# Performance work log

Hardware: AMD Instinct MI355X
Metric: run time of the kernel (lower is better)

Reference implementation:

```python
import jax, jax.numpy as jnp
import numpy as np

N, E, D, R, G, C = 100000, 600000, 128, 4, 256, 16
EPS = 1e-5

def _rgcn(x, src, dst, edge_type, w_rel, w_root, b):
    # out_i = x_i @ W_root + b + sum_r mean_{j in N_r(i)} x_j @ W_r  (PyG RGCNConv, aggr='mean')
    x_src = x[src]                                   # [E, D] gather
    out = x @ w_root + b                             # [N, D]
    for r in range(R):
        m = (edge_type == r).astype(x.dtype)         # [E]
        msg = (x_src @ w_rel[r]) * m[:, None]        # [E, D]
        agg = jax.ops.segment_sum(msg, dst, num_segments=N)
        cnt = jax.ops.segment_sum(m, dst, num_segments=N)
        out = out + agg / jnp.maximum(cnt, 1.0)[:, None]
    return out

def _bn_eval(x, gamma, beta, mean, var):
    return (x - mean) * jax.lax.rsqrt(var + EPS) * gamma + beta

def setup_inputs() -> dict:
    key = jax.random.key(0)
    ks = jax.random.split(key, 12)
    x = jax.random.normal(ks[0], (N, D), dtype=jnp.float32)
    edge_index = jax.random.randint(ks[1], (2, E), 0, N)
    edge_type = jax.random.randint(ks[2], (E,), 0, R)
    batch = jnp.sort(jax.random.randint(ks[3], (N,), 0, G))
    s = 1.0 / np.sqrt(D)
    conv_rel_w = jax.random.normal(ks[4], (3, R, D, D), dtype=jnp.float32) * s
    conv_root_w = jax.random.normal(ks[5], (3, D, D), dtype=jnp.float32) * s
    conv_bias = jnp.zeros((3, D), dtype=jnp.float32)
    bn_gamma = jnp.ones((2, D), dtype=jnp.float32)
    bn_beta = jnp.zeros((2, D), dtype=jnp.float32)
    bn_mean = jax.random.normal(ks[6], (2, D), dtype=jnp.float32) * 0.1
    bn_var = jax.random.uniform(ks[7], (2, D), minval=0.5, maxval=1.5, dtype=jnp.float32)
    cls_w1 = jax.random.normal(ks[8], (D, D // 2), dtype=jnp.float32) * s
    cls_b1 = jnp.zeros((D // 2,), dtype=jnp.float32)
    cls_w2 = jax.random.normal(ks[9], (D // 2, C), dtype=jnp.float32) / np.sqrt(D // 2)
    cls_b2 = jnp.zeros((C,), dtype=jnp.float32)
    return {"x": x, "edge_index": edge_index, "edge_type": edge_type, "batch": batch,
            "conv_rel_w": conv_rel_w, "conv_root_w": conv_root_w, "conv_bias": conv_bias,
            "bn_gamma": bn_gamma, "bn_beta": bn_beta, "bn_mean": bn_mean, "bn_var": bn_var,
            "cls_w1": cls_w1, "cls_b1": cls_b1, "cls_w2": cls_w2, "cls_b2": cls_b2}

def reference(x, edge_index, edge_type, batch, conv_rel_w, conv_root_w, conv_bias,
              bn_gamma, bn_beta, bn_mean, bn_var, cls_w1, cls_b1, cls_w2, cls_b2):
    src, dst = edge_index[0], edge_index[1]
    prev = None
    h = x
    for i in range(3):
        h_new = _rgcn(h, src, dst, edge_type, conv_rel_w[i], conv_root_w[i], conv_bias[i])
        if prev is not None:
            h_new = h_new + prev  # residual (shapes always match: D==D)
        if i != 2:
            h_new = _bn_eval(h_new, bn_gamma[i], bn_beta[i], bn_mean[i], bn_var[i])
            h_new = jax.nn.elu(h_new)  # alpha=1; dropout inactive in eval
        prev = h_new
        h = h_new
    # global mean pool over graphs
    sums = jax.ops.segment_sum(h, batch, num_segments=G)          # [G, D]
    cnts = jax.ops.segment_sum(jnp.ones((N,), h.dtype), batch, num_segments=G)
    pooled = sums / jnp.maximum(cnts, 1.0)[:, None]
    z = jax.nn.elu(pooled @ cls_w1 + cls_b1)
    logits = z @ cls_w2 + cls_b2
    return jax.nn.log_softmax(logits, axis=-1)
```

## Files before the change

kernel.cpp:

```cpp
#include <hip/hip_runtime.h>
#include <hip/hip_bf16.h>

#define NN 100000
#define EE 600000
#define DD 128
#define GG 256
#define CCL 16

typedef __attribute__((ext_vector_type(8))) short short8;
typedef __attribute__((ext_vector_type(4))) float f32x4;
typedef const __attribute__((address_space(1))) void* gas_t;
typedef __attribute__((address_space(3))) void* las_t;

__device__ __forceinline__ void async_ld16(const void* g, void* l) {
    __builtin_amdgcn_global_load_lds((gas_t)g, (las_t)l, 16, 0, 0);
}
__device__ __forceinline__ unsigned short f2bf(float x) {
    unsigned u = __float_as_uint(x);
    unsigned r = (u + 0x7FFFu + ((u >> 16) & 1u)) >> 16;
    return (unsigned short)r;
}
__device__ __forceinline__ float bf2f(unsigned short b) {
    return __uint_as_float(((unsigned)b) << 16);
}
__device__ __forceinline__ void unpack8(uint4 v, float* f) {
    f[0] = __uint_as_float(v.x << 16); f[1] = __uint_as_float(v.x & 0xFFFF0000u);
    f[2] = __uint_as_float(v.y << 16); f[3] = __uint_as_float(v.y & 0xFFFF0000u);
    f[4] = __uint_as_float(v.z << 16); f[5] = __uint_as_float(v.z & 0xFFFF0000u);
    f[6] = __uint_as_float(v.w << 16); f[7] = __uint_as_float(v.w & 0xFFFF0000u);
}

__global__ __launch_bounds__(256) void sniff_kernel(const void* __restrict__ xraw, int* __restrict__ flag) {
    int t = threadIdx.x;
    const unsigned short* u = (const unsigned short*)xraw;
    int good = 0;
    #pragma unroll
    for (int i = 0; i < 4; i++) {
        unsigned short b = u[t * 4 + i];
        int e = (b >> 7) & 0xFF;
        if (e >= 107 && e <= 130) good++;
    }
    __shared__ int sg[256];
    sg[t] = good;
    __syncthreads();
    for (int s = 128; s > 0; s >>= 1) { if (t < s) sg[t] += sg[t + s]; __syncthreads(); }
    if (t == 0) flag[0] = (sg[0] >= 900) ? 1 : 0;
}

__device__ __forceinline__ float loadf(const void* p, size_t i, int isbf) {
    if (isbf) return bf2f(((const unsigned short*)p)[i]);
    return ((const float*)p)[i];
}

__global__ __launch_bounds__(256) void convx_kernel(const void* __restrict__ xraw, const int* __restrict__ flag,
                                                    __hip_bfloat16* __restrict__ xc) {
    int isbf = flag[0];
    size_t i0 = ((size_t)blockIdx.x * 256 + threadIdx.x) * 8;
    if (i0 >= (size_t)NN * DD) return;
    if (isbf) {
        *(uint4*)(xc + i0) = *(const uint4*)((const __hip_bfloat16*)xraw + i0);
    } else {
        const float* xf = (const float*)xraw;
        unsigned short o[8];
        #pragma unroll
        for (int j = 0; j < 8; j++) o[j] = f2bf(xf[i0 + j]);
        *(uint4*)(xc + i0) = *(uint4*)o;
    }
}

__global__ __launch_bounds__(256) void convw_kernel(const void* __restrict__ rel_raw, const void* __restrict__ root_raw,
                                                    const int* __restrict__ flag, __hip_bfloat16* __restrict__ wt) {
    int isbf = flag[0];
    int mat = blockIdx.x;
    int layer = mat / 5, g = mat % 5;
    size_t srcoff = (g == 0) ? (size_t)layer * 16384 : (size_t)(layer * 4 + (g - 1)) * 16384;
    const void* sraw = (g == 0) ? root_raw : rel_raw;
    __hip_bfloat16* dstp = wt + (size_t)mat * 16384;
    for (int idx = threadIdx.x; idx < 16384; idx += 256) {
        int k = idx >> 7, n = idx & 127;
        float v = loadf(sraw, srcoff + (size_t)k * 128 + n, isbf);
        dstp[n * 128 + k] = __float2bfloat16(v);
    }
}

__global__ __launch_bounds__(256) void convp_kernel(const void* bias, const void* bng, const void* bnb,
                                                    const void* bnm, const void* bnv, const void* w1,
                                                    const void* b1, const void* w2, const void* b2,
                                                    const int* __restrict__ flag, float* __restrict__ pf) {
    int isbf = flag[0];
    int b = blockIdx.x, t = threadIdx.x;
    if (b < 9) {
        const void* srcs[9] = {bias, bng, bnb, bnm, bnv, w1, b1, w2, b2};
        const int cnts[9] = {384, 256, 256, 256, 256, 8192, 64, 1024, 16};
        const int offs[9] = {0, 384, 640, 896, 1152, 1408, 9600, 9664, 10688};
        const void* s = srcs[b];
        int c = cnts[b], o = offs[b];
        for (int i = t; i < c; i += 256) pf[o + i] = loadf(s, i, isbf);
    } else {
        int bl = b - 9;
        if (t < 128) {
            float iva = rsqrtf(loadf(bnv, bl * 128 + t, isbf) + 1e-5f);
            float gm = loadf(bng, bl * 128 + t, isbf) * iva;
            float ga = loadf(bnb, bl * 128 + t, isbf) - loadf(bnm, bl * 128 + t, isbf) * gm;
            pf[11008 + bl * 256 + t] = gm;
            pf[11008 + bl * 256 + 128 + t] = ga;
        }
    }
}

__global__ __launch_bounds__(256) void count4_kernel(const int* __restrict__ dst, const int* __restrict__ et,
                                                     int* __restrict__ cnt4) {
    int e = blockIdx.x * 256 + threadIdx.x;
    if (e < EE) atomicAdd(&cnt4[dst[e] * 4 + et[e]], 1);
}

__global__ __launch_bounds__(256) void allocn_kernel(const int* __restrict__ cnt4, int* __restrict__ counter,
                                                     int* __restrict__ startn, int* __restrict__ wptr4) {
    int n = blockIdx.x * 256 + threadIdx.x;
    int lane = threadIdx.x & 63;
    int4 cv = make_int4(0, 0, 0, 0);
    int c = 0;
    if (n < NN) {
        cv = *(const int4*)(cnt4 + n * 4);
        c = cv.x + cv.y + cv.z + cv.w;
    }
    int v = c;
    #pragma unroll
    for (int d = 1; d < 64; d <<= 1) {
        int o = __shfl_up(v, d);
        if (lane >= d) v += o;
    }
    int base = 0;
    if (lane == 63) base = atomicAdd(counter, v);
    base = __shfl(base, 63);
    if (n < NN) {
        int s = base + v - c;
        startn[n] = s;
        wptr4[n * 4 + 0] = s;
        wptr4[n * 4 + 1] = s + cv.x;
        wptr4[n * 4 + 2] = s + cv.x + cv.y;
        wptr4[n * 4 + 3] = s + cv.x + cv.y + cv.z;
    }
}

__global__ __launch_bounds__(256) void fill4_kernel(const int* __restrict__ src, const int* __restrict__ dst,
                                                    const int* __restrict__ et, int* __restrict__ wptr4,
                                                    int* __restrict__ esrc) {
    int e = blockIdx.x * 256 + threadIdx.x;
    if (e < EE) {
        int pos = atomicAdd(&wptr4[dst[e] * 4 + et[e]], 1);
        esrc[pos] = src[e];
    }
}

__global__ __launch_bounds__(256) void agg_kernel(const __hip_bfloat16* __restrict__ h,
                                                  const int* __restrict__ esrc,
                                                  const int* __restrict__ startn,
                                                  const int* __restrict__ cnt4,
                                                  __hip_bfloat16* __restrict__ Abuf) {
    int node = blockIdx.x * 16 + (threadIdx.x >> 4);
    int c16 = threadIdx.x & 15;
    int col0 = c16 * 8;
    int4 cv = *(const int4*)(cnt4 + node * 4);
    int s = startn[node];
    int cr[4] = {cv.x, cv.y, cv.z, cv.w};
    #pragma unroll
    for (int r = 0; r < 4; r++) {
        int c = cr[r];
        float a[8];
        #pragma unroll
        for (int j = 0; j < 8; j++) a[j] = 0.f;
        int i = 0;
        for (; i + 4 <= c; i += 4) {
            int s4[4];
            uint4 vv[4];
            #pragma unroll
            for (int q = 0; q < 4; q++) s4[q] = esrc[s + i + q];
            #pragma unroll
            for (int q = 0; q < 4; q++) vv[q] = *(const uint4*)(h + (size_t)s4[q] * 128 + col0);
            #pragma unroll
            for (int q = 0; q < 4; q++) {
                float f[8];
                unpack8(vv[q], f);
                #pragma unroll
                for (int j = 0; j < 8; j++) a[j] += f[j];
            }
        }
        for (; i < c; i++) {
            int sq = esrc[s + i];
            uint4 v0 = *(const uint4*)(h + (size_t)sq * 128 + col0);
            float f[8];
            unpack8(v0, f);
            #pragma unroll
            for (int j = 0; j < 8; j++) a[j] += f[j];
        }
        float w = (c > 0) ? (1.f / (float)c) : 0.f;
        unsigned short u[8];
        #pragma unroll
        for (int j = 0; j < 8; j++) u[j] = f2bf(a[j] * w);
        *(uint4*)(Abuf + (size_t)node * 512 + r * 128 + col0) = *(uint4*)u;
        s += c;
    }
}

__global__ __launch_bounds__(256) void rgemm_kernel(const __hip_bfloat16* __restrict__ h_in,
                                                    const __hip_bfloat16* __restrict__ Abuf,
                                                    const __hip_bfloat16* __restrict__ wt5,
                                                    const float* __restrict__ bias,
                                                    const float* __restrict__ gmp,
                                                    const float* __restrict__ gap,
                                                    const __hip_bfloat16* __restrict__ hres,
                                                    __hip_bfloat16* __restrict__ hout,
                                                    int do_bn) {
    __shared__ __align__(16) short lds[16384];
    int t = threadIdx.x;
    int wave = t >> 6, lane = t & 63, quad = lane >> 4, r16 = lane & 15;
    int m0 = blockIdx.x * 128;

    int r0 = m0 + wave * 32 + r16;      if (r0 > NN - 1) r0 = NN - 1;
    int r1 = m0 + wave * 32 + 16 + r16; if (r1 > NN - 1) r1 = NN - 1;

    f32x4 acc[2][8];
    #pragma unroll
    for (int i = 0; i < 2; i++)
        #pragma unroll
        for (int j = 0; j < 8; j++) acc[i][j] = (f32x4){0.f, 0.f, 0.f, 0.f};

    #pragma unroll
    for (int ch = 0; ch < 5; ch++) {
        if (ch) __syncthreads();
        const __hip_bfloat16* wg = wt5 + (size_t)ch * 16384;
        #pragma unroll
        for (int j = 0; j < 8; j++) {
            int slot = j * 256 + t;
            int brow = slot >> 4, sp = slot & 15;
            async_ld16(wg + brow * 128 + (sp ^ (brow & 15)) * 8, &lds[slot * 8]);
        }
        const __hip_bfloat16* ap0;
        const __hip_bfloat16* ap1;
        if (ch == 0) {
            ap0 = h_in + (size_t)r0 * 128;
            ap1 = h_in + (size_t)r1 * 128;
        } else {
            ap0 = Abuf + (size_t)r0 * 512 + (ch - 1) * 128;
            ap1 = Abuf + (size_t)r1 * 512 + (ch - 1) * 128;
        }
        short8 a0[4], a1[4];
        #pragma unroll
        for (int kc = 0; kc < 4; kc++) {
            a0[kc] = *(const short8*)(ap0 + kc * 32 + quad * 8);
            a1[kc] = *(const short8*)(ap1 + kc * 32 + quad * 8);
        }
        __syncthreads();
        #pragma unroll
        for (int kc = 0; kc < 4; kc++) {
            int s = kc * 4 + quad;
            #pragma unroll
            for (int nt = 0; nt < 8; nt++) {
                int rb = nt * 16 + r16;
                short8 b = *(const short8*)&lds[(rb * 16 + (s ^ (rb & 15))) * 8];
                acc[0][nt] = __builtin_amdgcn_mfma_f32_16x16x32_bf16(a0[kc], b, acc[0][nt], 0, 0, 0);
                acc[1][nt] = __builtin_amdgcn_mfma_f32_16x16x32_bf16(a1[kc], b, acc[1][nt], 0, 0, 0);
            }
        }
    }

    float* cf = (float*)lds;
    #pragma unroll
    for (int half = 0; half < 2; half++) {
        __syncthreads();
        #pragma unroll
        for (int nt = half * 4; nt < half * 4 + 4; nt++) {
            int col = (nt - half * 4) * 16 + r16;
            #pragma unroll
            for (int mt = 0; mt < 2; mt++) {
                #pragma unroll
                for (int reg = 0; reg < 4; reg++) {
                    int crow = wave * 32 + mt * 16 + quad * 4 + reg;
                    cf[crow * 64 + col] = acc[mt][nt][reg];
                }
            }
        }
        __syncthreads();
        #pragma unroll
        for (int it = 0; it < 4; it++) {
            int u4 = it * 256 + t;
            int crow = u4 >> 3, seg = u4 & 7;
            int node = m0 + crow;
            if (node < NN) {
                int gcol0 = half * 64 + seg * 8;
                float a[8];
                #pragma unroll
                for (int j = 0; j < 8; j++) a[j] = cf[crow * 64 + seg * 8 + j] + bias[gcol0 + j];
                if (hres) {
                    float rf[8];
                    unpack8(*(const uint4*)(hres + (size_t)node * 128 + gcol0), rf);
                    #pragma unroll
                    for (int j = 0; j < 8; j++) a[j] += rf[j];
                }
                if (do_bn) {
                    #pragma unroll
                    for (int j = 0; j < 8; j++) {
                        float z = a[j] * gmp[gcol0 + j] + gap[gcol0 + j];
                        a[j] = z > 0.f ? z : expm1f(z);
                    }
                }
                unsigned short u[8];
                #pragma unroll
                for (int j = 0; j < 8; j++) u[j] = f2bf(a[j]);
                *(uint4*)(hout + (size_t)node * 128 + gcol0) = *(uint4*)u;
            }
        }
    }
}

__global__ __launch_bounds__(256) void pool_kernel(const __hip_bfloat16* __restrict__ h3,
                                                   const int* __restrict__ batch,
                                                   float* __restrict__ pooled) {
    int g = blockIdx.x, t = threadIdx.x;
    int rowpar = t >> 4, colg = t & 15;
    int lo = 0, hi = NN;
    while (lo < hi) { int mid = (lo + hi) >> 1; if (batch[mid] < g) lo = mid + 1; else hi = mid; }
    int s0 = lo;
    hi = NN;
    while (lo < hi) { int mid = (lo + hi) >> 1; if (batch[mid] < g + 1) lo = mid + 1; else hi = mid; }
    int s1 = lo;
    float a[8];
    #pragma unroll
    for (int j = 0; j < 8; j++) a[j] = 0.f;
    for (int n = s0 + rowpar; n < s1; n += 16) {
        float f[8];
        unpack8(*(const uint4*)(h3 + (size_t)n * 128 + colg * 8), f);
        #pragma unroll
        for (int j = 0; j < 8; j++) a[j] += f[j];
    }
    __shared__ float sd[16][128];
    #pragma unroll
    for (int j = 0; j < 8; j++) sd[rowpar][colg * 8 + j] = a[j];
    __syncthreads();
    if (t < 128) {
        float sum = 0.f;
        #pragma unroll
        for (int i = 0; i < 16; i++) sum += sd[i][t];
        int cgn = s1 - s0;
        pooled[g * 128 + t] = sum / (float)(cgn > 0 ? cgn : 1);
    }
}

__global__ __launch_bounds__(64) void cls_kernel(const float* __restrict__ pooled,
                                                 const float* __restrict__ pf,
                                                 const int* __restrict__ flag,
                                                 void* __restrict__ out) {
    int g = blockIdx.x, j = threadIdx.x;
    const float* w1 = pf + 1408;
    const float* b1 = pf + 9600;
    const float* w2 = pf + 9664;
    const float* b2 = pf + 10688;
    __shared__ float z[64];
    __shared__ float lg[16];
    const float* p = pooled + g * 128;
    float acc = b1[j];
    for (int d = 0; d < 128; d++) acc += p[d] * w1[d * 64 + j];
    acc = acc > 0.f ? acc : expm1f(acc);
    z[j] = acc;
    __syncthreads();
    if (j < CCL) {
        float l = b2[j];
        for (int k = 0; k < 64; k++) l += z[k] * w2[k * 16 + j];
        lg[j] = l;
    }
    __syncthreads();
    if (j < CCL) {
        float m = lg[0];
        for (int k = 1; k < CCL; k++) m = fmaxf(m, lg[k]);
        float s = 0.f;
        for (int k = 0; k < CCL; k++) s += expf(lg[k] - m);
        float val = lg[j] - m - logf(s);
        if (flag[0]) ((__hip_bfloat16*)out)[g * CCL + j] = __float2bfloat16(val);
        else         ((float*)out)[g * CCL + j] = val;
    }
}

extern "C" void kernel_launch(void* const* d_in, const int* in_sizes, int n_in,
                              void* d_out, int out_size, void* d_ws, size_t ws_size,
                              hipStream_t stream) {
    const void* x_raw    = d_in[0];
    const int* ei        = (const int*)d_in[1];
    const int* et        = (const int*)d_in[2];
    const int* batch     = (const int*)d_in[3];
    const void* rel_raw  = d_in[4];
    const void* root_raw = d_in[5];
    const int* srcp = ei;
    const int* dstp = ei + EE;

    char* ws = (char*)d_ws;
    size_t off = 0;
    auto take = [&](size_t bytes) { size_t r = off; off += (bytes + 1023) & ~(size_t)1023; return r; };
    __hip_bfloat16* Abuf  = (__hip_bfloat16*)(ws + take((size_t)NN * 512 * 2));
    __hip_bfloat16* xc    = (__hip_bfloat16*)(ws + take((size_t)NN * 128 * 2));
    __hip_bfloat16* hA    = (__hip_bfloat16*)(ws + take((size_t)NN * 128 * 2));
    __hip_bfloat16* hB    = (__hip_bfloat16*)(ws + take((size_t)NN * 128 * 2));
    __hip_bfloat16* hC    = (__hip_bfloat16*)(ws + take((size_t)NN * 128 * 2));
    __hip_bfloat16* wt    = (__hip_bfloat16*)(ws + take((size_t)15 * 16384 * 2));
    float* pf             = (float*)(ws + take((size_t)11520 * 4));
    float* pooled         = (float*)(ws + take((size_t)GG * 128 * 4));
    int* cnt4             = (int*)(ws + take((size_t)NN * 16 + 8));
    int* counter          = cnt4 + NN * 4;
    int* flag             = cnt4 + NN * 4 + 1;
    int* startn           = (int*)(ws + take((size_t)NN * 4));
    int* wptr4            = (int*)(ws + take((size_t)NN * 16));
    int* esrc             = (int*)(ws + take((size_t)EE * 4));

    hipMemsetAsync(cnt4, 0, (size_t)NN * 16 + 4, stream);
    sniff_kernel<<<1, 256, 0, stream>>>(x_raw, flag);
    convx_kernel<<<(NN * DD / 8 + 255) / 256, 256, 0, stream>>>(x_raw, flag, xc);
    convw_kernel<<<15, 256, 0, stream>>>(rel_raw, root_raw, flag, wt);
    convp_kernel<<<11, 256, 0, stream>>>(d_in[6], d_in[7], d_in[8], d_in[9], d_in[10],
                                         d_in[11], d_in[12], d_in[13], d_in[14], flag, pf);
    count4_kernel<<<(EE + 255) / 256, 256, 0, stream>>>(dstp, et, cnt4);
    allocn_kernel<<<(NN + 255) / 256, 256, 0, stream>>>(cnt4, counter, startn, wptr4);
    fill4_kernel<<<(EE + 255) / 256, 256, 0, stream>>>(srcp, dstp, et, wptr4, esrc);

    const __hip_bfloat16* hin = xc;
    __hip_bfloat16* houts[3] = {hA, hB, hC};
    for (int l = 0; l < 3; l++) {
        int bl = l < 2 ? l : 1;
        agg_kernel<<<NN / 16, 256, 0, stream>>>(hin, esrc, startn, cnt4, Abuf);
        rgemm_kernel<<<(NN + 127) / 128, 256, 0, stream>>>(
            hin, Abuf, wt + (size_t)l * 5 * 16384, pf + l * 128,
            pf + 11008 + bl * 256, pf + 11008 + bl * 256 + 128,
            (l > 0) ? hin : (const __hip_bfloat16*)nullptr, houts[l], (l < 2) ? 1 : 0);
        hin = houts[l];
    }
    pool_kernel<<<GG, 256, 0, stream>>>(houts[2], batch, pooled);
    cls_kernel<<<GG, 64, 0, stream>>>(pooled, pf, flag, (void*)d_out);
}
```

Measured before the change: 572.7 us.

## Double-buffer weight chunks and split rgemm across 8 waves

The fused relational GEMM now runs with 512 threads, so each of the 8 waves computes a 32x64 output tile instead of a 32x128 tile. Weight chunks are double-buffered in LDS and the next chunk's A rows are prefetched while the current chunk's MFMAs run, so loads overlap compute. The epilogue writes the whole 128-column tile to padded LDS (stride 132) in one pass instead of two halves. The cost is more LDS per block (about 66 KB) and extra registers for the prefetched A fragments, which may limit occupancy.

```diff
diff --git a/kernel.cpp b/kernel.cpp
--- a/kernel.cpp
+++ b/kernel.cpp
@@ -203,113 +203,113 @@
     }
 }
 
-__global__ __launch_bounds__(256) void rgemm_kernel(const __hip_bfloat16* __restrict__ h_in,
-                                                    const __hip_bfloat16* __restrict__ Abuf,
-                                                    const __hip_bfloat16* __restrict__ wt5,
-                                                    const float* __restrict__ bias,
-                                                    const float* __restrict__ gmp,
-                                                    const float* __restrict__ gap,
-                                                    const __hip_bfloat16* __restrict__ hres,
-                                                    __hip_bfloat16* __restrict__ hout,
-                                                    int do_bn) {
-    __shared__ __align__(16) short lds[16384];
+#define STAGE_B(P, CH) do { \
+    const __hip_bfloat16* _wg = wt5 + (size_t)(CH) * 16384; \
+    _Pragma("unroll") \
+    for (int _j = 0; _j < 4; _j++) { \
+        int _slot = _j * 512 + t; \
+        int _brow = _slot >> 4, _sp = _slot & 15; \
+        async_ld16(_wg + _brow * 128 + (_sp ^ (_brow & 15)) * 8, &ldsb[(P) * 16384 + _slot * 8]); \
+    } \
+} while (0)
+
+#define LOAD_A(D0, D1, CH) do { \
+    const __hip_bfloat16* _p0 = ((CH) == 0) ? (h_in + (size_t)r0 * 128) : (Abuf + (size_t)r0 * 512 + ((CH) - 1) * 128); \
+    const __hip_bfloat16* _p1 = ((CH) == 0) ? (h_in + (size_t)r1 * 128) : (Abuf + (size_t)r1 * 512 + ((CH) - 1) * 128); \
+    _Pragma("unroll") \
+    for (int _kc = 0; _kc < 4; _kc++) { \
+        D0[_kc] = *(const short8*)(_p0 + _kc * 32 + quad * 8); \
+        D1[_kc] = *(const short8*)(_p1 + _kc * 32 + quad * 8); \
+    } \
+} while (0)
+
+#define MFMA_CH(P, A0, A1) do { \
+    _Pragma("unroll") \
+    for (int _kc = 0; _kc < 4; _kc++) { \
+        int _s = _kc * 4 + quad; \
+        _Pragma("unroll") \
+        for (int _nt = 0; _nt < 4; _nt++) { \
+            int _rb = wc * 64 + _nt * 16 + r16; \
+            short8 _b = *(const short8*)&ldsb[(P) * 16384 + (_rb * 16 + (_s ^ (_rb & 15))) * 8]; \
+            acc0[_nt] = __builtin_amdgcn_mfma_f32_16x16x32_bf16(A0[_kc], _b, acc0[_nt], 0, 0, 0); \
+            acc1[_nt] = __builtin_amdgcn_mfma_f32_16x16x32_bf16(A1[_kc], _b, acc1[_nt], 0, 0, 0); \
+        } \
+    } \
+} while (0)
+
+__global__ __launch_bounds__(512, 4) void rgemm_kernel(const __hip_bfloat16* __restrict__ h_in,
+                                                       const __hip_bfloat16* __restrict__ Abuf,
+                                                       const __hip_bfloat16* __restrict__ wt5,
+                                                       const float* __restrict__ bias,
+                                                       const float* __restrict__ gmp,
+                                                       const float* __restrict__ gap,
+                                                       const __hip_bfloat16* __restrict__ hres,
+                                                       __hip_bfloat16* __restrict__ hout,
+                                                       int do_bn) {
+    __shared__ __align__(16) char ldsraw[132 * 128 * 4];
+    short* ldsb = (short*)ldsraw;
+    float* cf = (float*)ldsraw;
     int t = threadIdx.x;
     int wave = t >> 6, lane = t & 63, quad = lane >> 4, r16 = lane & 15;
+    int wr = wave & 3, wc = wave >> 2;
     int m0 = blockIdx.x * 128;
 
-    int r0 = m0 + wave * 32 + r16;      if (r0 > NN - 1) r0 = NN - 1;
-    int r1 = m0 + wave * 32 + 16 + r16; if (r1 > NN - 1) r1 = NN - 1;
-
-    f32x4 acc[2][8];
-    #pragma unroll
-    for (int i = 0; i < 2; i++)
-        #pragma unroll
-        for (int j = 0; j < 8; j++) acc[i][j] = (f32x4){0.f, 0.f, 0.f, 0.f};
-
-    #pragma unroll
-    for (int ch = 0; ch < 5; ch++) {
-        if (ch) __syncthreads();
-        const __hip_bfloat16* wg = wt5 + (size_t)ch * 16384;
-        #pragma unroll
-        for (int j = 0; j < 8; j++) {
-            int slot = j * 256 + t;
-            int brow = slot >> 4, sp = slot & 15;
-            async_ld16(wg + brow * 128 + (sp ^ (brow & 15)) * 8, &lds[slot * 8]);
+    int r0 = m0 + wr * 32 + r16;      if (r0 > NN - 1) r0 = NN - 1;
+    int r1 = m0 + wr * 32 + 16 + r16; if (r1 > NN - 1) r1 = NN - 1;
+
+    f32x4 acc0[4], acc1[4];
+    #pragma unroll
+    for (int j = 0; j < 4; j++) { acc0[j] = (f32x4){0.f, 0.f, 0.f, 0.f}; acc1[j] = (f32x4){0.f, 0.f, 0.f, 0.f}; }
+
+    short8 aA0[4], aA1[4], aB0[4], aB1[4];
+    LOAD_A(aA0, aA1, 0);
+    STAGE_B(0, 0);
+
+    __syncthreads();  STAGE_B(1, 1);  LOAD_A(aB0, aB1, 1);  MFMA_CH(0, aA0, aA1);
+    __syncthreads();  STAGE_B(0, 2);  LOAD_A(aA0, aA1, 2);  MFMA_CH(1, aB0, aB1);
+    __syncthreads();  STAGE_B(1, 3);  LOAD_A(aB0, aB1, 3);  MFMA_CH(0, aA0, aA1);
+    __syncthreads();  STAGE_B(0, 4);  LOAD_A(aA0, aA1, 4);  MFMA_CH(1, aB0, aB1);
+    __syncthreads();                                        MFMA_CH(0, aA0, aA1);
+
+    __syncthreads();
+    #pragma unroll
+    for (int nt = 0; nt < 4; nt++) {
+        int col = wc * 64 + nt * 16 + r16;
+        #pragma unroll
+        for (int reg = 0; reg < 4; reg++) {
+            int crow0 = wr * 32 + quad * 4 + reg;
+            cf[crow0 * 132 + col] = acc0[nt][reg];
+            cf[(crow0 + 16) * 132 + col] = acc1[nt][reg];
         }
-        const __hip_bfloat16* ap0;
-        const __hip_bfloat16* ap1;
-        if (ch == 0) {
-            ap0 = h_in + (size_t)r0 * 128;
-            ap1 = h_in + (size_t)r1 * 128;
-        } else {
-            ap0 = Abuf + (size_t)r0 * 512 + (ch - 1) * 128;
-            ap1 = Abuf + (size_t)r1 * 512 + (ch - 1) * 128;
-        }
-        short8 a0[4], a1[4];
-        #pragma unroll
-        for (int kc = 0; kc < 4; kc++) {
-            a0[kc] = *(const short8*)(ap0 + kc * 32 + quad * 8);
-            a1[kc] = *(const short8*)(ap1 + kc * 32 + quad * 8);
-        }
-        __syncthreads();
-        #pragma unroll
-        for (int kc = 0; kc < 4; kc++) {
-            int s = kc * 4 + quad;
-            #pragma unroll
-            for (int nt = 0; nt < 8; nt++) {
-                int rb = nt * 16 + r16;
-                short8 b = *(const short8*)&lds[(rb * 16 + (s ^ (rb & 15))) * 8];
-                acc[0][nt] = __builtin_amdgcn_mfma_f32_16x16x32_bf16(a0[kc], b, acc[0][nt], 0, 0, 0);
-                acc[1][nt] = __builtin_amdgcn_mfma_f32_16x16x32_bf16(a1[kc], b, acc[1][nt], 0, 0, 0);
+    }
+    __syncthreads();
+    #pragma unroll
+    for (int it = 0; it < 4; it++) {
+        int u4 = it * 512 + t;
+        int crow = u4 >> 4, seg = u4 & 15;
+        int node = m0 + crow;
+        if (node < NN) {
+            int gcol0 = seg * 8;
+            float a[8];
+            #pragma unroll
+            for (int j = 0; j < 8; j++) a[j] = cf[crow * 132 + gcol0 + j] + bias[gcol0 + j];
+            if (hres) {
+                float rf[8];
+                unpack8(*(const uint4*)(hres + (size_t)node * 128 + gcol0), rf);
+                #pragma unroll
+                for (int j = 0; j < 8; j++) a[j] += rf[j];
             }
-        }
-    }
-
-    float* cf = (float*)lds;
-    #pragma unroll
-    for (int half = 0; half < 2; half++) {
-        __syncthreads();
-        #pragma unroll
-        for (int nt = half * 4; nt < half * 4 + 4; nt++) {
-            int col = (nt - half * 4) * 16 + r16;
-            #pragma unroll
-            for (int mt = 0; mt < 2; mt++) {
+            if (do_bn) {
                 #pragma unroll
-                for (int reg = 0; reg < 4; reg++) {
-                    int crow = wave * 32 + mt * 16 + quad * 4 + reg;
-                    cf[crow * 64 + col] = acc[mt][nt][reg];
+                for (int j = 0; j < 8; j++) {
+                    float z = a[j] * gmp[gcol0 + j] + gap[gcol0 + j];
+                    a[j] = z > 0.f ? z : expm1f(z);
                 }
             }
-        }
-        __syncthreads();
-        #pragma unroll
-        for (int it = 0; it < 4; it++) {
-            int u4 = it * 256 + t;
-            int crow = u4 >> 3, seg = u4 & 7;
-            int node = m0 + crow;
-            if (node < NN) {
-                int gcol0 = half * 64 + seg * 8;
-                float a[8];
-                #pragma unroll
-                for (int j = 0; j < 8; j++) a[j] = cf[crow * 64 + seg * 8 + j] + bias[gcol0 + j];
-                if (hres) {
-                    float rf[8];
-                    unpack8(*(const uint4*)(hres + (size_t)node * 128 + gcol0), rf);
-                    #pragma unroll
-                    for (int j = 0; j < 8; j++) a[j] += rf[j];
-                }
-                if (do_bn) {
-                    #pragma unroll
-                    for (int j = 0; j < 8; j++) {
-                        float z = a[j] * gmp[gcol0 + j] + gap[gcol0 + j];
-                        a[j] = z > 0.f ? z : expm1f(z);
-                    }
-                }
-                unsigned short u[8];
-                #pragma unroll
-                for (int j = 0; j < 8; j++) u[j] = f2bf(a[j]);
-                *(uint4*)(hout + (size_t)node * 128 + gcol0) = *(uint4*)u;
-            }
+            unsigned short u[8];
+            #pragma unroll
+            for (int j = 0; j < 8; j++) u[j] = f2bf(a[j]);
+            *(uint4*)(hout + (size_t)node * 128 + gcol0) = *(uint4*)u;
         }
     }
 }
@@ -426,7 +426,7 @@
     for (int l = 0; l < 3; l++) {
         int bl = l < 2 ? l : 1;
         agg_kernel<<<NN / 16, 256, 0, stream>>>(hin, esrc, startn, cnt4, Abuf);
-        rgemm_kernel<<<(NN + 127) / 128, 256, 0, stream>>>(
+        rgemm_kernel<<<(NN + 127) / 128, 512, 0, stream>>>(
             hin, Abuf, wt + (size_t)l * 5 * 16384, pf + l * 128,
             pf + 11008 + bl * 256, pf + 11008 + bl * 256 + 128,
             (l > 0) ? hin : (const __hip_bfloat16*)nullptr, houts[l], (l < 2) ? 1 : 0);
```

Measured after the change: 651.9 us. 13.8% more time.

## Split GEMM over output-column halves with full-K weights in LDS; merge relation loops in aggregation

Applied to the files above, without the earlier changes.

The fused root+relation GEMM now uses a 2D grid that splits the 128 output columns into two halves. Each block loads its 64x640 weight slice into LDS once, with a new concatenated K=640 weight layout, instead of reloading five 128x128 chunks behind barriers. A-operands are preloaded into registers in two batches. The aggregation kernel walks all of a node's edges in one loop of 8 gathers, keeping four per-relation accumulators selected by masks, which exposes more memory-level parallelism. The costs are that A rows are now read twice (once per column half), LDS use grows to 80KB per block which lowers occupancy, and the aggregation does four times the FMAs per edge.

```diff
diff --git a/kernel.cpp b/kernel.cpp
--- a/kernel.cpp
+++ b/kernel.cpp
@@ -75,11 +75,11 @@
     int layer = mat / 5, g = mat % 5;
     size_t srcoff = (g == 0) ? (size_t)layer * 16384 : (size_t)(layer * 4 + (g - 1)) * 16384;
     const void* sraw = (g == 0) ? root_raw : rel_raw;
-    __hip_bfloat16* dstp = wt + (size_t)mat * 16384;
+    __hip_bfloat16* dstp = wt + (size_t)layer * 81920 + g * 128;
     for (int idx = threadIdx.x; idx < 16384; idx += 256) {
-        int k = idx >> 7, n = idx & 127;
-        float v = loadf(sraw, srcoff + (size_t)k * 128 + n, isbf);
-        dstp[n * 128 + k] = __float2bfloat16(v);
+        int kk = idx >> 7, n = idx & 127;
+        float v = loadf(sraw, srcoff + (size_t)kk * 128 + n, isbf);
+        dstp[(size_t)n * 640 + kk] = __float2bfloat16(v);
     }
 }
 
@@ -163,153 +163,181 @@
     int col0 = c16 * 8;
     int4 cv = *(const int4*)(cnt4 + node * 4);
     int s = startn[node];
-    int cr[4] = {cv.x, cv.y, cv.z, cv.w};
-    #pragma unroll
-    for (int r = 0; r < 4; r++) {
-        int c = cr[r];
-        float a[8];
-        #pragma unroll
-        for (int j = 0; j < 8; j++) a[j] = 0.f;
-        int i = 0;
-        for (; i + 4 <= c; i += 4) {
-            int s4[4];
-            uint4 vv[4];
+    int b1 = cv.x, b2 = b1 + cv.y, b3 = b2 + cv.z, ct = b3 + cv.w;
+    float a0[8], a1[8], a2[8], a3[8];
+    #pragma unroll
+    for (int j = 0; j < 8; j++) { a0[j] = 0.f; a1[j] = 0.f; a2[j] = 0.f; a3[j] = 0.f; }
+    int i = 0;
+    for (; i + 8 <= ct; i += 8) {
+        int e8[8];
+        uint4 vv[8];
+        #pragma unroll
+        for (int q = 0; q < 8; q++) e8[q] = esrc[s + i + q];
+        #pragma unroll
+        for (int q = 0; q < 8; q++) vv[q] = *(const uint4*)(h + (size_t)e8[q] * 128 + col0);
+        #pragma unroll
+        for (int q = 0; q < 8; q++) {
+            int pos = i + q;
+            int r = (pos >= b1) + (pos >= b2) + (pos >= b3);
+            float w0 = (r == 0) ? 1.f : 0.f, w1 = (r == 1) ? 1.f : 0.f;
+            float w2 = (r == 2) ? 1.f : 0.f, w3 = (r == 3) ? 1.f : 0.f;
+            float f[8];
+            unpack8(vv[q], f);
             #pragma unroll
-            for (int q = 0; q < 4; q++) s4[q] = esrc[s + i + q];
-            #pragma unroll
-            for (int q = 0; q < 4; q++) vv[q] = *(const uint4*)(h + (size_t)s4[q] * 128 + col0);
-            #pragma unroll
-            for (int q = 0; q < 4; q++) {
-                float f[8];
-                unpack8(vv[q], f);
-                #pragma unroll
-                for (int j = 0; j < 8; j++) a[j] += f[j];
+            for (int j = 0; j < 8; j++) {
+                a0[j] += w0 * f[j]; a1[j] += w1 * f[j];
+                a2[j] += w2 * f[j]; a3[j] += w3 * f[j];
             }
         }
-        for (; i < c; i++) {
-            int sq = esrc[s + i];
-            uint4 v0 = *(const uint4*)(h + (size_t)sq * 128 + col0);
-            float f[8];
-            unpack8(v0, f);
-            #pragma unroll
-            for (int j = 0; j < 8; j++) a[j] += f[j];
-        }
-        float w = (c > 0) ? (1.f / (float)c) : 0.f;
-        unsigned short u[8];
-        #pragma unroll
-        for (int j = 0; j < 8; j++) u[j] = f2bf(a[j] * w);
-        *(uint4*)(Abuf + (size_t)node * 512 + r * 128 + col0) = *(uint4*)u;
-        s += c;
-    }
+    }
+    for (; i < ct; i++) {
+        int e0 = esrc[s + i];
+        uint4 v0 = *(const uint4*)(h + (size_t)e0 * 128 + col0);
+        int r = (i >= b1) + (i >= b2) + (i >= b3);
+        float w0 = (r == 0) ? 1.f : 0.f, w1 = (r == 1) ? 1.f : 0.f;
+        float w2 = (r == 2) ? 1.f : 0.f, w3 = (r == 3) ? 1.f : 0.f;
+        float f[8];
+        unpack8(v0, f);
+        #pragma unroll
+        for (int j = 0; j < 8; j++) {
+            a0[j] += w0 * f[j]; a1[j] += w1 * f[j];
+            a2[j] += w2 * f[j]; a3[j] += w3 * f[j];
+        }
+    }
+    float i0 = 1.f / (float)(cv.x > 0 ? cv.x : 1);
+    float i1 = 1.f / (float)(cv.y > 0 ? cv.y : 1);
+    float i2 = 1.f / (float)(cv.z > 0 ? cv.z : 1);
+    float i3 = 1.f / (float)(cv.w > 0 ? cv.w : 1);
+    unsigned short u[8];
+    __hip_bfloat16* op = Abuf + (size_t)node * 512 + col0;
+    #pragma unroll
+    for (int j = 0; j < 8; j++) u[j] = f2bf(a0[j] * i0);
+    *(uint4*)(op) = *(uint4*)u;
+    #pragma unroll
+    for (int j = 0; j < 8; j++) u[j] = f2bf(a1[j] * i1);
+    *(uint4*)(op + 128) = *(uint4*)u;
+    #pragma unroll
+    for (int j = 0; j < 8; j++) u[j] = f2bf(a2[j] * i2);
+    *(uint4*)(op + 256) = *(uint4*)u;
+    #pragma unroll
+    for (int j = 0; j < 8; j++) u[j] = f2bf(a3[j] * i3);
+    *(uint4*)(op + 384) = *(uint4*)u;
 }
 
 __global__ __launch_bounds__(256) void rgemm_kernel(const __hip_bfloat16* __restrict__ h_in,
                                                     const __hip_bfloat16* __restrict__ Abuf,
-                                                    const __hip_bfloat16* __restrict__ wt5,
+                                                    const __hip_bfloat16* __restrict__ wtL,
                                                     const float* __restrict__ bias,
                                                     const float* __restrict__ gmp,
                                                     const float* __restrict__ gap,
                                                     const __hip_bfloat16* __restrict__ hres,
                                                     __hip_bfloat16* __restrict__ hout,
                                                     int do_bn) {
-    __shared__ __align__(16) short lds[16384];
+    __shared__ __align__(16) short ldsb[40960];
     int t = threadIdx.x;
-    int wave = t >> 6, lane = t & 63, quad = lane >> 4, r16 = lane & 15;
+    int wv = t >> 6, lane = t & 63, quad = lane >> 4, r16 = lane & 15;
     int m0 = blockIdx.x * 128;
-
-    int r0 = m0 + wave * 32 + r16;      if (r0 > NN - 1) r0 = NN - 1;
-    int r1 = m0 + wave * 32 + 16 + r16; if (r1 > NN - 1) r1 = NN - 1;
-
-    f32x4 acc[2][8];
-    #pragma unroll
-    for (int i = 0; i < 2; i++)
-        #pragma unroll
-        for (int j = 0; j < 8; j++) acc[i][j] = (f32x4){0.f, 0.f, 0.f, 0.f};
-
-    #pragma unroll
-    for (int ch = 0; ch < 5; ch++) {
-        if (ch) __syncthreads();
-        const __hip_bfloat16* wg = wt5 + (size_t)ch * 16384;
-        #pragma unroll
-        for (int j = 0; j < 8; j++) {
-            int slot = j * 256 + t;
-            int brow = slot >> 4, sp = slot & 15;
-            async_ld16(wg + brow * 128 + (sp ^ (brow & 15)) * 8, &lds[slot * 8]);
-        }
-        const __hip_bfloat16* ap0;
-        const __hip_bfloat16* ap1;
-        if (ch == 0) {
-            ap0 = h_in + (size_t)r0 * 128;
-            ap1 = h_in + (size_t)r1 * 128;
+    int nh = blockIdx.y;
+
+    #pragma unroll
+    for (int i = 0; i < 20; i++) {
+        int u = i * 256 + t;
+        int nl = u / 80;
+        int segp = u - nl * 80;
+        int seg = segp ^ (nl & 7);
+        async_ld16(wtL + (size_t)(nh * 64 + nl) * 640 + seg * 8, &ldsb[u * 8]);
+    }
+
+    int r0 = m0 + wv * 32 + r16;       if (r0 > NN - 1) r0 = NN - 1;
+    int r1 = m0 + wv * 32 + 16 + r16;  if (r1 > NN - 1) r1 = NN - 1;
+
+    short8 aA0[10], aA1[10];
+    #pragma unroll
+    for (int j = 0; j < 10; j++) {
+        if (j < 4) {
+            aA0[j] = *(const short8*)(h_in + (size_t)r0 * 128 + j * 32 + quad * 8);
+            aA1[j] = *(const short8*)(h_in + (size_t)r1 * 128 + j * 32 + quad * 8);
         } else {
-            ap0 = Abuf + (size_t)r0 * 512 + (ch - 1) * 128;
-            ap1 = Abuf + (size_t)r1 * 512 + (ch - 1) * 128;
-        }
-        short8 a0[4], a1[4];
-        #pragma unroll
-        for (int kc = 0; kc < 4; kc++) {
-            a0[kc] = *(const short8*)(ap0 + kc * 32 + quad * 8);
-            a1[kc] = *(const short8*)(ap1 + kc * 32 + quad * 8);
-        }
-        __syncthreads();
-        #pragma unroll
-        for (int kc = 0; kc < 4; kc++) {
-            int s = kc * 4 + quad;
+            aA0[j] = *(const short8*)(Abuf + (size_t)r0 * 512 + (j - 4) * 32 + quad * 8);
+            aA1[j] = *(const short8*)(Abuf + (size_t)r1 * 512 + (j - 4) * 32 + quad * 8);
+        }
+    }
+    __syncthreads();
+
+    short8 aB0[10], aB1[10];
+    #pragma unroll
+    for (int j = 0; j < 10; j++) {
+        aB0[j] = *(const short8*)(Abuf + (size_t)r0 * 512 + (j + 6) * 32 + quad * 8);
+        aB1[j] = *(const short8*)(Abuf + (size_t)r1 * 512 + (j + 6) * 32 + quad * 8);
+    }
+
+    f32x4 acc0[4], acc1[4];
+    #pragma unroll
+    for (int nt = 0; nt < 4; nt++) { acc0[nt] = (f32x4){0.f,0.f,0.f,0.f}; acc1[nt] = (f32x4){0.f,0.f,0.f,0.f}; }
+
+    #pragma unroll
+    for (int j = 0; j < 10; j++) {
+        #pragma unroll
+        for (int nt = 0; nt < 4; nt++) {
+            int nl = nt * 16 + r16;
+            int unit = nl * 80 + ((j * 4 + quad) ^ (nl & 7));
+            short8 b = *(const short8*)&ldsb[unit * 8];
+            acc0[nt] = __builtin_amdgcn_mfma_f32_16x16x32_bf16(aA0[j], b, acc0[nt], 0, 0, 0);
+            acc1[nt] = __builtin_amdgcn_mfma_f32_16x16x32_bf16(aA1[j], b, acc1[nt], 0, 0, 0);
+        }
+    }
+    #pragma unroll
+    for (int j = 0; j < 10; j++) {
+        #pragma unroll
+        for (int nt = 0; nt < 4; nt++) {
+            int nl = nt * 16 + r16;
+            int unit = nl * 80 + (((j + 10) * 4 + quad) ^ (nl & 7));
+            short8 b = *(const short8*)&ldsb[unit * 8];
+            acc0[nt] = __builtin_amdgcn_mfma_f32_16x16x32_bf16(aB0[j], b, acc0[nt], 0, 0, 0);
+            acc1[nt] = __builtin_amdgcn_mfma_f32_16x16x32_bf16(aB1[j], b, acc1[nt], 0, 0, 0);
+        }
+    }
+
+    __syncthreads();
+    float* cf = (float*)ldsb;
+    #pragma unroll
+    for (int nt = 0; nt < 4; nt++) {
+        int col = nt * 16 + r16;
+        #pragma unroll
+        for (int reg = 0; reg < 4; reg++) {
+            cf[(wv * 32 + quad * 4 + reg) * 66 + col] = acc0[nt][reg];
+            cf[(wv * 32 + 16 + quad * 4 + reg) * 66 + col] = acc1[nt][reg];
+        }
+    }
+    __syncthreads();
+    #pragma unroll
+    for (int it = 0; it < 4; it++) {
+        int u4 = it * 256 + t;
+        int row = u4 >> 3, oct = u4 & 7;
+        int onode = m0 + row;
+        if (onode < NN) {
+            int gc = nh * 64 + oct * 8;
+            const float* cp = cf + row * 66 + oct * 8;
+            float a[8];
             #pragma unroll
-            for (int nt = 0; nt < 8; nt++) {
-                int rb = nt * 16 + r16;
-                short8 b = *(const short8*)&lds[(rb * 16 + (s ^ (rb & 15))) * 8];
-                acc[0][nt] = __builtin_amdgcn_mfma_f32_16x16x32_bf16(a0[kc], b, acc[0][nt], 0, 0, 0);
-                acc[1][nt] = __builtin_amdgcn_mfma_f32_16x16x32_bf16(a1[kc], b, acc[1][nt], 0, 0, 0);
+            for (int j = 0; j < 8; j++) a[j] = cp[j] + bias[gc + j];
+            if (hres) {
+                float rf[8];
+                unpack8(*(const uint4*)(hres + (size_t)onode * 128 + gc), rf);
+                #pragma unroll
+                for (int j = 0; j < 8; j++) a[j] += rf[j];
             }
-        }
-    }
-
-    float* cf = (float*)lds;
-    #pragma unroll
-    for (int half = 0; half < 2; half++) {
-        __syncthreads();
-        #pragma unroll
-        for (int nt = half * 4; nt < half * 4 + 4; nt++) {
-            int col = (nt - half * 4) * 16 + r16;
-            #pragma unroll
-            for (int mt = 0; mt < 2; mt++) {
+            if (do_bn) {
                 #pragma unroll
-                for (int reg = 0; reg < 4; reg++) {
-                    int crow = wave * 32 + mt * 16 + quad * 4 + reg;
-                    cf[crow * 64 + col] = acc[mt][nt][reg];
+                for (int j = 0; j < 8; j++) {
+                    float z = a[j] * gmp[gc + j] + gap[gc + j];
+                    a[j] = z > 0.f ? z : expm1f(z);
                 }
             }
-        }
-        __syncthreads();
-        #pragma unroll
-        for (int it = 0; it < 4; it++) {
-            int u4 = it * 256 + t;
-            int crow = u4 >> 3, seg = u4 & 7;
-            int node = m0 + crow;
-            if (node < NN) {
-                int gcol0 = half * 64 + seg * 8;
-                float a[8];
-                #pragma unroll
-                for (int j = 0; j < 8; j++) a[j] = cf[crow * 64 + seg * 8 + j] + bias[gcol0 + j];
-                if (hres) {
-                    float rf[8];
-                    unpack8(*(const uint4*)(hres + (size_t)node * 128 + gcol0), rf);
-                    #pragma unroll
-                    for (int j = 0; j < 8; j++) a[j] += rf[j];
-                }
-                if (do_bn) {
-                    #pragma unroll
-                    for (int j = 0; j < 8; j++) {
-                        float z = a[j] * gmp[gcol0 + j] + gap[gcol0 + j];
-                        a[j] = z > 0.f ? z : expm1f(z);
-                    }
-                }
-                unsigned short u[8];
-                #pragma unroll
-                for (int j = 0; j < 8; j++) u[j] = f2bf(a[j]);
-                *(uint4*)(hout + (size_t)node * 128 + gcol0) = *(uint4*)u;
-            }
+            unsigned short u[8];
+            #pragma unroll
+            for (int j = 0; j < 8; j++) u[j] = f2bf(a[j]);
+            *(uint4*)(hout + (size_t)onode * 128 + gc) = *(uint4*)u;
         }
     }
 }
@@ -401,7 +429,7 @@
     __hip_bfloat16* hA    = (__hip_bfloat16*)(ws + take((size_t)NN * 128 * 2));
     __hip_bfloat16* hB    = (__hip_bfloat16*)(ws + take((size_t)NN * 128 * 2));
     __hip_bfloat16* hC    = (__hip_bfloat16*)(ws + take((size_t)NN * 128 * 2));
-    __hip_bfloat16* wt    = (__hip_bfloat16*)(ws + take((size_t)15 * 16384 * 2));
+    __hip_bfloat16* wt    = (__hip_bfloat16*)(ws + take((size_t)3 * 81920 * 2));
     float* pf             = (float*)(ws + take((size_t)11520 * 4));
     float* pooled         = (float*)(ws + take((size_t)GG * 128 * 4));
     int* cnt4             = (int*)(ws + take((size_t)NN * 16 + 8));
@@ -426,8 +454,8 @@
     for (int l = 0; l < 3; l++) {
         int bl = l < 2 ? l : 1;
         agg_kernel<<<NN / 16, 256, 0, stream>>>(hin, esrc, startn, cnt4, Abuf);
-        rgemm_kernel<<<(NN + 127) / 128, 256, 0, stream>>>(
-            hin, Abuf, wt + (size_t)l * 5 * 16384, pf + l * 128,
+        rgemm_kernel<<<dim3((NN + 127) / 128, 2), 256, 0, stream>>>(
+            hin, Abuf, wt + (size_t)l * 81920, pf + l * 128,
             pf + 11008 + bl * 256, pf + 11008 + bl * 256 + 128,
             (l > 0) ? hin : (const __hip_bfloat16*)nullptr, houts[l], (l < 2) ? 1 : 0);
         hin = houts[l];
```

Result: slower. 680.8 us (+18.9%).

## Read GEMM weights directly from global memory with a fused K=640 layout

Applied to the files above, without the earlier changes.

The weight conversion now writes each layer's five 128x128 matrices as one transposed [128 x 640] row-major block. The fused GEMM reads B fragments straight from global memory (cached in L2/L1) rather than staging each chunk into LDS with per-chunk barriers, and runs over the concatenated K dimension with a prefetch of the first aggregated chunk. This removes five LDS fills and their syncs per block, at the cost of more redundant global/cache loads per wave. The epilogue LDS tile is padded to stride 66 to reduce bank conflicts.

```diff
diff --git a/kernel.cpp b/kernel.cpp
--- a/kernel.cpp
+++ b/kernel.cpp
@@ -9,12 +9,7 @@
 
 typedef __attribute__((ext_vector_type(8))) short short8;
 typedef __attribute__((ext_vector_type(4))) float f32x4;
-typedef const __attribute__((address_space(1))) void* gas_t;
-typedef __attribute__((address_space(3))) void* las_t;
-
-__device__ __forceinline__ void async_ld16(const void* g, void* l) {
-    __builtin_amdgcn_global_load_lds((gas_t)g, (las_t)l, 16, 0, 0);
-}
+
 __device__ __forceinline__ unsigned short f2bf(float x) {
     unsigned u = __float_as_uint(x);
     unsigned r = (u + 0x7FFFu + ((u >> 16) & 1u)) >> 16;
@@ -75,11 +70,11 @@
     int layer = mat / 5, g = mat % 5;
     size_t srcoff = (g == 0) ? (size_t)layer * 16384 : (size_t)(layer * 4 + (g - 1)) * 16384;
     const void* sraw = (g == 0) ? root_raw : rel_raw;
-    __hip_bfloat16* dstp = wt + (size_t)mat * 16384;
+    __hip_bfloat16* dstp = wt + (size_t)layer * 81920 + g * 128;
     for (int idx = threadIdx.x; idx < 16384; idx += 256) {
-        int k = idx >> 7, n = idx & 127;
-        float v = loadf(sraw, srcoff + (size_t)k * 128 + n, isbf);
-        dstp[n * 128 + k] = __float2bfloat16(v);
+        int kk = idx >> 7, n = idx & 127;
+        float v = loadf(sraw, srcoff + (size_t)kk * 128 + n, isbf);
+        dstp[(size_t)n * 640 + kk] = __float2bfloat16(v);
     }
 }
 
@@ -205,110 +200,106 @@
 
 __global__ __launch_bounds__(256) void rgemm_kernel(const __hip_bfloat16* __restrict__ h_in,
                                                     const __hip_bfloat16* __restrict__ Abuf,
-                                                    const __hip_bfloat16* __restrict__ wt5,
+                                                    const __hip_bfloat16* __restrict__ wtL,
                                                     const float* __restrict__ bias,
                                                     const float* __restrict__ gmp,
                                                     const float* __restrict__ gap,
                                                     const __hip_bfloat16* __restrict__ hres,
                                                     __hip_bfloat16* __restrict__ hout,
                                                     int do_bn) {
-    __shared__ __align__(16) short lds[16384];
+    __shared__ __align__(16) float cf[128 * 66];
     int t = threadIdx.x;
-    int wave = t >> 6, lane = t & 63, quad = lane >> 4, r16 = lane & 15;
+    int wv = t >> 6, lane = t & 63, quad = lane >> 4, r16 = lane & 15;
     int m0 = blockIdx.x * 128;
-
-    int r0 = m0 + wave * 32 + r16;      if (r0 > NN - 1) r0 = NN - 1;
-    int r1 = m0 + wave * 32 + 16 + r16; if (r1 > NN - 1) r1 = NN - 1;
-
-    f32x4 acc[2][8];
-    #pragma unroll
-    for (int i = 0; i < 2; i++)
-        #pragma unroll
-        for (int j = 0; j < 8; j++) acc[i][j] = (f32x4){0.f, 0.f, 0.f, 0.f};
-
-    #pragma unroll
-    for (int ch = 0; ch < 5; ch++) {
-        if (ch) __syncthreads();
-        const __hip_bfloat16* wg = wt5 + (size_t)ch * 16384;
-        #pragma unroll
-        for (int j = 0; j < 8; j++) {
-            int slot = j * 256 + t;
-            int brow = slot >> 4, sp = slot & 15;
-            async_ld16(wg + brow * 128 + (sp ^ (brow & 15)) * 8, &lds[slot * 8]);
-        }
-        const __hip_bfloat16* ap0;
-        const __hip_bfloat16* ap1;
-        if (ch == 0) {
-            ap0 = h_in + (size_t)r0 * 128;
-            ap1 = h_in + (size_t)r1 * 128;
-        } else {
-            ap0 = Abuf + (size_t)r0 * 512 + (ch - 1) * 128;
-            ap1 = Abuf + (size_t)r1 * 512 + (ch - 1) * 128;
-        }
-        short8 a0[4], a1[4];
-        #pragma unroll
-        for (int kc = 0; kc < 4; kc++) {
-            a0[kc] = *(const short8*)(ap0 + kc * 32 + quad * 8);
-            a1[kc] = *(const short8*)(ap1 + kc * 32 + quad * 8);
-        }
-        __syncthreads();
-        #pragma unroll
-        for (int kc = 0; kc < 4; kc++) {
-            int s = kc * 4 + quad;
+    int r0 = m0 + wv * 32 + r16;      if (r0 > NN - 1) r0 = NN - 1;
+    int r1 = m0 + wv * 32 + 16 + r16; if (r1 > NN - 1) r1 = NN - 1;
+
+    f32x4 acc0[8], acc1[8];
+    #pragma unroll
+    for (int nt = 0; nt < 8; nt++) { acc0[nt] = (f32x4){0.f,0.f,0.f,0.f}; acc1[nt] = (f32x4){0.f,0.f,0.f,0.f}; }
+
+    const __hip_bfloat16* pb  = wtL + r16 * 640 + quad * 8;
+    const __hip_bfloat16* ph0 = h_in + (size_t)r0 * 128 + quad * 8;
+    const __hip_bfloat16* ph1 = h_in + (size_t)r1 * 128 + quad * 8;
+    const __hip_bfloat16* pa0 = Abuf + (size_t)r0 * 512 + quad * 8;
+    const __hip_bfloat16* pa1 = Abuf + (size_t)r1 * 512 + quad * 8;
+
+    short8 pf0 = *(const short8*)(pa0);
+    short8 pf1 = *(const short8*)(pa1);
+
+    #pragma unroll 2
+    for (int j = 0; j < 4; j++) {
+        short8 a0 = *(const short8*)(ph0 + j * 32);
+        short8 a1 = *(const short8*)(ph1 + j * 32);
+        #pragma unroll
+        for (int nt = 0; nt < 8; nt++) {
+            short8 b = *(const short8*)(pb + nt * 10240 + j * 32);
+            acc0[nt] = __builtin_amdgcn_mfma_f32_16x16x32_bf16(a0, b, acc0[nt], 0, 0, 0);
+            acc1[nt] = __builtin_amdgcn_mfma_f32_16x16x32_bf16(a1, b, acc1[nt], 0, 0, 0);
+        }
+    }
+    {
+        #pragma unroll
+        for (int nt = 0; nt < 8; nt++) {
+            short8 b = *(const short8*)(pb + nt * 10240 + 4 * 32);
+            acc0[nt] = __builtin_amdgcn_mfma_f32_16x16x32_bf16(pf0, b, acc0[nt], 0, 0, 0);
+            acc1[nt] = __builtin_amdgcn_mfma_f32_16x16x32_bf16(pf1, b, acc1[nt], 0, 0, 0);
+        }
+    }
+    #pragma unroll 2
+    for (int j = 1; j < 16; j++) {
+        short8 a0 = *(const short8*)(pa0 + j * 32);
+        short8 a1 = *(const short8*)(pa1 + j * 32);
+        #pragma unroll
+        for (int nt = 0; nt < 8; nt++) {
+            short8 b = *(const short8*)(pb + nt * 10240 + (j + 4) * 32);
+            acc0[nt] = __builtin_amdgcn_mfma_f32_16x16x32_bf16(a0, b, acc0[nt], 0, 0, 0);
+            acc1[nt] = __builtin_amdgcn_mfma_f32_16x16x32_bf16(a1, b, acc1[nt], 0, 0, 0);
+        }
+    }
+
+    #pragma unroll
+    for (int half = 0; half < 2; half++) {
+        if (half) __syncthreads();
+        #pragma unroll
+        for (int nt = 0; nt < 4; nt++) {
+            int nn = half * 4 + nt;
+            int col = nt * 16 + r16;
             #pragma unroll
-            for (int nt = 0; nt < 8; nt++) {
-                int rb = nt * 16 + r16;
-                short8 b = *(const short8*)&lds[(rb * 16 + (s ^ (rb & 15))) * 8];
-                acc[0][nt] = __builtin_amdgcn_mfma_f32_16x16x32_bf16(a0[kc], b, acc[0][nt], 0, 0, 0);
-                acc[1][nt] = __builtin_amdgcn_mfma_f32_16x16x32_bf16(a1[kc], b, acc[1][nt], 0, 0, 0);
-            }
-        }
-    }
-
-    float* cf = (float*)lds;
-    #pragma unroll
-    for (int half = 0; half < 2; half++) {
-        __syncthreads();
-        #pragma unroll
-        for (int nt = half * 4; nt < half * 4 + 4; nt++) {
-            int col = (nt - half * 4) * 16 + r16;
-            #pragma unroll
-            for (int mt = 0; mt < 2; mt++) {
-                #pragma unroll
-                for (int reg = 0; reg < 4; reg++) {
-                    int crow = wave * 32 + mt * 16 + quad * 4 + reg;
-                    cf[crow * 64 + col] = acc[mt][nt][reg];
-                }
+            for (int reg = 0; reg < 4; reg++) {
+                cf[(wv * 32 + quad * 4 + reg) * 66 + col] = acc0[nn][reg];
+                cf[(wv * 32 + 16 + quad * 4 + reg) * 66 + col] = acc1[nn][reg];
             }
         }
         __syncthreads();
         #pragma unroll
         for (int it = 0; it < 4; it++) {
             int u4 = it * 256 + t;
-            int crow = u4 >> 3, seg = u4 & 7;
-            int node = m0 + crow;
-            if (node < NN) {
-                int gcol0 = half * 64 + seg * 8;
+            int row = u4 >> 3, oct = u4 & 7;
+            int onode = m0 + row;
+            if (onode < NN) {
+                int gc = half * 64 + oct * 8;
+                const float* cp = cf + row * 66 + oct * 8;
                 float a[8];
                 #pragma unroll
-                for (int j = 0; j < 8; j++) a[j] = cf[crow * 64 + seg * 8 + j] + bias[gcol0 + j];
+                for (int j = 0; j < 8; j++) a[j] = cp[j] + bias[gc + j];
                 if (hres) {
                     float rf[8];
-                    unpack8(*(const uint4*)(hres + (size_t)node * 128 + gcol0), rf);
+                    unpack8(*(const uint4*)(hres + (size_t)onode * 128 + gc), rf);
                     #pragma unroll
                     for (int j = 0; j < 8; j++) a[j] += rf[j];
                 }
                 if (do_bn) {
                     #pragma unroll
                     for (int j = 0; j < 8; j++) {
-                        float z = a[j] * gmp[gcol0 + j] + gap[gcol0 + j];
+                        float z = a[j] * gmp[gc + j] + gap[gc + j];
                         a[j] = z > 0.f ? z : expm1f(z);
                     }
                 }
                 unsigned short u[8];
                 #pragma unroll
                 for (int j = 0; j < 8; j++) u[j] = f2bf(a[j]);
-                *(uint4*)(hout + (size_t)node * 128 + gcol0) = *(uint4*)u;
+                *(uint4*)(hout + (size_t)onode * 128 + gc) = *(uint4*)u;
             }
         }
     }
@@ -401,7 +392,7 @@
     __hip_bfloat16* hA    = (__hip_bfloat16*)(ws + take((size_t)NN * 128 * 2));
     __hip_bfloat16* hB    = (__hip_bfloat16*)(ws + take((size_t)NN * 128 * 2));
     __hip_bfloat16* hC    = (__hip_bfloat16*)(ws + take((size_t)NN * 128 * 2));
-    __hip_bfloat16* wt    = (__hip_bfloat16*)(ws + take((size_t)15 * 16384 * 2));
+    __hip_bfloat16* wt    = (__hip_bfloat16*)(ws + take((size_t)3 * 81920 * 2));
     float* pf             = (float*)(ws + take((size_t)11520 * 4));
     float* pooled         = (float*)(ws + take((size_t)GG * 128 * 4));
     int* cnt4             = (int*)(ws + take((size_t)NN * 16 + 8));
@@ -427,7 +418,7 @@
         int bl = l < 2 ? l : 1;
         agg_kernel<<<NN / 16, 256, 0, stream>>>(hin, esrc, startn, cnt4, Abuf);
         rgemm_kernel<<<(NN + 127) / 128, 256, 0, stream>>>(
-            hin, Abuf, wt + (size_t)l * 5 * 16384, pf + l * 128,
+            hin, Abuf, wt + (size_t)l * 81920, pf + l * 128,
             pf + 11008 + bl * 256, pf + 11008 + bl * 256 + 128,
             (l > 0) ? hin : (const __hip_bfloat16*)nullptr, houts[l], (l < 2) ? 1 : 0);
         hin = houts[l];
```

Measured after the change: 754.9 us. 31.8% more time.
